# Kernel optimization log

Measured on AMD Instinct MI355X. Metric: run time of the kernel, lower is better.

Reference implementation:

```python
import jax, jax.numpy as jnp
import numpy as np

N, D, C = 4096, 512, 128
TOPK = 12  # rank-0 hard neg + up to 11 fallback ranks (torch loop breaks at loop_cnt>=10 -> max rank 11)


def setup_inputs() -> dict:
    key = jax.random.key(0)
    k1, k2, k3, k4, k5 = jax.random.split(key, 5)
    return {
        "inputs": jax.random.normal(k1, (N, D), jnp.float32),
        "prediction": jax.random.normal(k2, (N, C), jnp.float32),
        "targets": jax.random.randint(k3, (N,), 0, C),
        "true_targets": jax.random.randint(k4, (N,), 0, C),
        "prob": jax.random.uniform(k5, (N,), jnp.float32),
        "threshold": jnp.float32(0.5),
    }


def _gumbel_argmax(key, mask):
    # uniform random choice over True entries of each row (Gumbel-max trick)
    g = jax.random.gumbel(key, mask.shape, jnp.float32)
    return jnp.argmax(jnp.where(mask, g, -jnp.inf), axis=1)


def reference(inputs, prediction, targets, true_targets, prob, threshold):
    margin = jnp.float32(0.3)
    n = inputs.shape[0]
    rows = jnp.arange(n)
    # pairwise euclidean distance: ||xi||^2 + ||xj||^2 - 2 xi.xj, clamp+sqrt
    sq = jnp.sum(inputs * inputs, axis=1)
    d2 = sq[:, None] + sq[None, :] - 2.0 * (inputs @ inputs.T)
    dist = jnp.sqrt(jnp.clip(d2, 1e-12))  # [n, n]

    eye = jnp.eye(n, dtype=bool)
    same = targets[:, None] == targets[None, :]
    is_neg = ~same
    conf = prob >= threshold  # is_confident per anchor

    key = jax.random.key(42)
    kp, kp2 = jax.random.split(key)

    # random positive (!= i) and hardest negative per row
    ap_idx = _gumbel_argmax(kp, same & ~eye)
    neg_dist = jnp.where(is_neg, dist, jnp.inf)
    an_idx = jnp.argmin(neg_dist, axis=1)

    ap0 = dist[rows, ap_idx]
    an0 = dist[rows, an_idx]
    pos_conf = prob[ap_idx] >= threshold
    neg_conf = prob[an_idx] >= threshold
    # false-negative test: hard neg predicted as anchor's (noisy) label
    is_fn = jnp.argmax(prediction[an_idx], axis=1) == targets

    # case B (pos conf, neg unconf, FN): walk ranked negs for first confident one (ranks 1..11)
    nv, ni = jax.lax.top_k(-neg_dist, TOPK)  # smallest TOPK neg distances
    cand_conf = prob[ni] >= threshold
    tail = cand_conf[:, 1:]
    found = jnp.any(tail, axis=1)
    r = jnp.where(found, 1 + jnp.argmax(tail, axis=1), TOPK - 1)
    an_B = dist[rows, ni[rows, r]]

    # cases C / D-notFN: resample a confident positive (!= i); fallback to original pos
    conf_pos = same & ~eye & (prob >= threshold)[None, :]
    new_pos = jnp.where(jnp.any(conf_pos, axis=1), _gumbel_argmax(kp2, conf_pos), ap_idx)
    ap_new = dist[rows, new_pos]

    caseB = pos_conf & ~neg_conf & is_fn
    swap = (~pos_conf) & (neg_conf | ~is_fn)  # case C or case D-notFN
    inverse = (~pos_conf) & (~neg_conf) & is_fn

    half = (ap0 + an0) * 0.5
    ap = jnp.where(caseB, half, jnp.where(swap, ap_new, ap0))
    an = jnp.where(caseB, an_B, jnp.where(swap, half, an0))

    row_loss = jnp.where(inverse,
                         jax.nn.relu(an - ap + margin),
                         jax.nn.relu(ap - an + margin))
    cnt = jnp.sum(conf)
    loss = jnp.sum(jnp.where(conf, row_loss, 0.0)) / jnp.maximum(cnt, 1).astype(jnp.float32)
    correct = jnp.sum((an >= ap) & conf)
    return loss, correct
```

## Files before the change

### kernel.cpp

```cpp
#include <hip/hip_runtime.h>
#include <stdint.h>
#include <math.h>

#define N_ 4096
#define D_ 512
#define C_ 128
#define MAXC 256

typedef __attribute__((ext_vector_type(8))) short bf16x8;
typedef __attribute__((ext_vector_type(4))) float f32x4;

__host__ __device__ __forceinline__ uint32_t rotl32_(uint32_t x, int d) {
  return (x << d) | (x >> (32 - d));
}
__host__ __device__ inline void tf2x32(uint32_t k0, uint32_t k1,
                                       uint32_t x0, uint32_t x1,
                                       uint32_t& y0, uint32_t& y1) {
  const uint32_t k2 = k0 ^ k1 ^ 0x1BD11BDAu;
#define TF_R(rr) { x0 += x1; x1 = rotl32_(x1, rr); x1 ^= x0; }
  x0 += k0; x1 += k1;
  TF_R(13) TF_R(15) TF_R(26) TF_R(6)
  x0 += k1; x1 += k2 + 1u;
  TF_R(17) TF_R(29) TF_R(16) TF_R(24)
  x0 += k2; x1 += k0 + 2u;
  TF_R(13) TF_R(15) TF_R(26) TF_R(6)
  x0 += k0; x1 += k1 + 3u;
  TF_R(17) TF_R(29) TF_R(16) TF_R(24)
  x0 += k1; x1 += k2 + 4u;
  TF_R(13) TF_R(15) TF_R(26) TF_R(6)
  x0 += k2; x1 += k0 + 5u;
#undef TF_R
  y0 = x0; y1 = x1;
}

__device__ __forceinline__ float gumbel_ij(uint32_t k0, uint32_t k1, uint32_t m) {
  uint32_t y0, y1;
  tf2x32(k0, k1, 0u, m, y0, y1);
  uint32_t bits = y0 ^ y1;
  uint32_t vb = (bits >> 9) | 0x3f800000u;
  float f = __uint_as_float(vb) - 1.0f;
  float u = (f == 0.0f) ? 1.1754943508222875e-38f : f;
  return -logf(-logf(u));
}

__device__ __forceinline__ unsigned short f2bf(float x) {
  unsigned int b = __float_as_uint(x);
  b += 0x7fffu + ((b >> 16) & 1u);
  return (unsigned short)(b >> 16);
}
__device__ __forceinline__ float bf2f(unsigned short u) {
  return __uint_as_float(((unsigned int)u) << 16);
}

__global__ void zero_k(float* __restrict__ accum, int* __restrict__ ccnt) {
  int t = threadIdx.x;
  if (t == 0) {
    accum[0] = 0.0f;
    ((unsigned*)accum)[1] = 0u;
    ((unsigned*)accum)[2] = 0u;
  }
  if (t < C_) ccnt[t] = 0;
}

__global__ __launch_bounds__(64) void prep_k(const float* __restrict__ inputs,
                                             const float* __restrict__ pred,
                                             const int* __restrict__ targets,
                                             float* __restrict__ sq,
                                             int* __restrict__ pam,
                                             int* __restrict__ ccnt,
                                             int* __restrict__ clist,
                                             unsigned short* __restrict__ XH,
                                             unsigned short* __restrict__ XL,
                                             int do_split, int do_list) {
  int i = blockIdx.x;
  int lane = threadIdx.x;
  const float4* rp = (const float4*)(inputs + (size_t)i * D_);
  float s = 0.0f;
#pragma unroll
  for (int q = 0; q < 2; ++q) {
    float4 v = rp[lane + 64 * q];
    s += v.x * v.x + v.y * v.y + v.z * v.z + v.w * v.w;
    if (do_split) {
      unsigned short h0 = f2bf(v.x), h1 = f2bf(v.y), h2 = f2bf(v.z), h3 = f2bf(v.w);
      unsigned short g0 = f2bf(v.x - bf2f(h0)), g1 = f2bf(v.y - bf2f(h1));
      unsigned short g2 = f2bf(v.z - bf2f(h2)), g3 = f2bf(v.w - bf2f(h3));
      uint2 hp, lp;
      hp.x = (unsigned)h0 | ((unsigned)h1 << 16); hp.y = (unsigned)h2 | ((unsigned)h3 << 16);
      lp.x = (unsigned)g0 | ((unsigned)g1 << 16); lp.y = (unsigned)g2 | ((unsigned)g3 << 16);
      size_t blk = ((size_t)(i >> 4) * 16 + ((lane >> 3) + 8 * q)) * 512;
      int lf = (i & 15) + 16 * ((lane & 7) >> 1);
      int j0 = 4 * (lane & 1);
      *(uint2*)&XH[blk + lf * 8 + j0] = hp;
      *(uint2*)&XL[blk + lf * 8 + j0] = lp;
    }
  }
#pragma unroll
  for (int off = 32; off; off >>= 1) s += __shfl_down(s, off);
  if (lane == 0) sq[i] = s;

  float v0 = pred[(size_t)i * C_ + lane];
  float v1 = pred[(size_t)i * C_ + 64 + lane];
  float bv; int bi;
  if (v1 > v0) { bv = v1; bi = lane + 64; } else { bv = v0; bi = lane; }
#pragma unroll
  for (int off = 32; off; off >>= 1) {
    float ov = __shfl_down(bv, off);
    int oi = __shfl_down(bi, off);
    if (ov > bv || (ov == bv && oi < bi)) { bv = ov; bi = oi; }
  }
  if (lane == 0) {
    pam[i] = bi;
    if (do_list) {
      int t = targets[i];
      int p = atomicAdd(&ccnt[t], 1);
      if (p < MAXC) clist[t * MAXC + p] = i;
    }
  }
}

__global__ __launch_bounds__(256, 2) void bigk4_k(const unsigned short* __restrict__ XH,
                                                  const unsigned short* __restrict__ XL,
                                                  const int* __restrict__ targets,
                                                  const float* __restrict__ sq,
                                                  float* __restrict__ pD,
                                                  int* __restrict__ pI) {
  __shared__ float U[8448];
  __shared__ float sqc[512];
  __shared__ int tcs[512];
  __shared__ float sqr[64];
  __shared__ int trs[64];

  const int tid = threadIdx.x, w = tid >> 6, l = tid & 63;
  const int rb = blockIdx.x >> 3, sl = blockIdx.x & 7;
  const int rbase = rb * 64, cbase0 = sl * 512;

  sqc[tid] = sq[cbase0 + tid]; sqc[tid + 256] = sq[cbase0 + 256 + tid];
  tcs[tid] = targets[cbase0 + tid]; tcs[tid + 256] = targets[cbase0 + 256 + tid];
  if (tid < 64) { sqr[tid] = sq[rbase + tid]; trs[tid] = targets[rbase + tid]; }

  const int lo = l * 8;
  size_t ta[4], tb[8];
#pragma unroll
  for (int rt = 0; rt < 4; ++rt) ta[rt] = (size_t)((rbase >> 4) + rt) * 8192;
#pragma unroll
  for (int c = 0; c < 8; ++c) tb[c] = (size_t)((cbase0 >> 4) + w * 8 + c) * 8192;

  f32x4 acc[4][8];
#pragma unroll
  for (int rt = 0; rt < 4; ++rt)
#pragma unroll
    for (int c = 0; c < 8; ++c) acc[rt][c] = (f32x4){0.f, 0.f, 0.f, 0.f};

  for (int kc = 0; kc < 16; ++kc) {
    const int off = kc * 512 + lo;
    bf16x8 ah[4], al_[4];
#pragma unroll
    for (int rt = 0; rt < 4; ++rt) {
      ah[rt] = *(const bf16x8*)(XH + ta[rt] + off);
      al_[rt] = *(const bf16x8*)(XL + ta[rt] + off);
    }
#pragma unroll
    for (int c = 0; c < 8; ++c) {
      bf16x8 bh = *(const bf16x8*)(XH + tb[c] + off);
      bf16x8 bl = *(const bf16x8*)(XL + tb[c] + off);
#pragma unroll
      for (int rt = 0; rt < 4; ++rt) {
        acc[rt][c] = __builtin_amdgcn_mfma_f32_16x16x32_bf16(ah[rt], bh, acc[rt][c], 0, 0, 0);
        acc[rt][c] = __builtin_amdgcn_mfma_f32_16x16x32_bf16(ah[rt], bl, acc[rt][c], 0, 0, 0);
        acc[rt][c] = __builtin_amdgcn_mfma_f32_16x16x32_bf16(al_[rt], bh, acc[rt][c], 0, 0, 0);
      }
    }
  }

  float* Dl = U;
  float dl[12]; int il[12];
#pragma unroll
  for (int q = 0; q < 12; ++q) { dl[q] = INFINITY; il[q] = 0; }
  const int srow = tid >> 2, scq = tid & 3;
  const int orow = (l >> 4) * 4;
  const int lr = l & 15;

  for (int g = 0; g < 4; ++g) {
    __syncthreads();
    if (w == g) {
#pragma unroll
      for (int rt = 0; rt < 4; ++rt)
#pragma unroll
        for (int c = 0; c < 8; ++c)
#pragma unroll
          for (int r = 0; r < 4; ++r) {
            int row = rt * 16 + orow + r;
            int cl = c * 16 + lr;
            float d2 = sqr[row] + sqc[g * 128 + cl] - 2.0f * acc[rt][c][r];
            float d = (trs[row] == tcs[g * 128 + cl]) ? INFINITY : sqrtf(fmaxf(d2, 1e-12f));
            Dl[row * 132 + cl] = d;
          }
    }
    __syncthreads();
    for (int q = 0; q < 32; ++q) {
      float d = Dl[srow * 132 + scq + 4 * q];
      if (d < dl[11]) {
        int col = cbase0 + g * 128 + scq + 4 * q;
        bool placed = false;
#pragma unroll
        for (int t = 11; t >= 1; --t) {
          if (!placed) {
            if (dl[t - 1] > d) { dl[t] = dl[t - 1]; il[t] = il[t - 1]; }
            else { dl[t] = d; il[t] = col; placed = true; }
          }
        }
        if (!placed) { dl[0] = d; il[0] = col; }
      }
    }
  }

  __syncthreads();
  float* MD = U;
  int* MI = (int*)(U + 3072);
#pragma unroll
  for (int q = 0; q < 12; ++q) { MD[tid * 12 + q] = dl[q]; MI[tid * 12 + q] = il[q]; }
  __syncthreads();
  if ((tid & 3) == 0) {
    int row = tid >> 2;
    int grow = rbase + row;
    float* outD = pD + ((size_t)grow * 8 + sl) * 12;
    int* outI = pI + ((size_t)grow * 8 + sl) * 12;
    int p0 = 0, p1 = 0, p2 = 0, p3 = 0;
    for (int o = 0; o < 12; ++o) {
      float bd = INFINITY; int bi = 0x7fffffff; int bc = 0;
      if (p0 < 12) { float d = MD[(row * 4 + 0) * 12 + p0]; int ix = MI[(row * 4 + 0) * 12 + p0]; if (d < bd || (d == bd && ix < bi)) { bd = d; bi = ix; bc = 0; } }
      if (p1 < 12) { float d = MD[(row * 4 + 1) * 12 + p1]; int ix = MI[(row * 4 + 1) * 12 + p1]; if (d < bd || (d == bd && ix < bi)) { bd = d; bi = ix; bc = 1; } }
      if (p2 < 12) { float d = MD[(row * 4 + 2) * 12 + p2]; int ix = MI[(row * 4 + 2) * 12 + p2]; if (d < bd || (d == bd && ix < bi)) { bd = d; bi = ix; bc = 2; } }
      if (p3 < 12) { float d = MD[(row * 4 + 3) * 12 + p3]; int ix = MI[(row * 4 + 3) * 12 + p3]; if (d < bd || (d == bd && ix < bi)) { bd = d; bi = ix; bc = 3; } }
      outD[o] = bd; outI[o] = bi;
      if (bc == 0) p0++; else if (bc == 1) p1++; else if (bc == 2) p2++; else p3++;
    }
  }
}

__global__ __launch_bounds__(256, 2) void bigk_k(const float* __restrict__ inputs,
                                                 const int* __restrict__ targets,
                                                 const float* __restrict__ sq,
                                                 float* __restrict__ pD,
                                                 int* __restrict__ pI) {
  __shared__ float U[10496];
  __shared__ float sqc[256];
  __shared__ int tcs[256];
  __shared__ float sqr[64];
  __shared__ int trs[64];

  float* Al = U;
  float* Bl = U + 2176;
  float* Dl = U;
  float* MD = U;
  int* MI = (int*)(U + 3072);

  const int tid = threadIdx.x;
  const int rb = blockIdx.x >> 3, sl = blockIdx.x & 7;
  const int rbase = rb * 64, cbase0 = sl * 512;

  if (tid < 64) { sqr[tid] = sq[rbase + tid]; trs[tid] = targets[rbase + tid]; }

  float dl[12]; int il[12];
#pragma unroll
  for (int q = 0; q < 12; ++q) { dl[q] = INFINITY; il[q] = 0; }

  const int w = tid >> 6, lane = tid & 63;
  const int rg = lane >> 3, cg = lane & 7;
  const int r0 = rg * 8, c0l = w * 64 + cg * 8;
  const int srow = tid >> 2, scq = tid & 3;

  for (int ci = 0; ci < 2; ++ci) {
    const int cbase = cbase0 + ci * 256;
    __syncthreads();
    sqc[tid] = sq[cbase + tid];
    tcs[tid] = targets[cbase + tid];

    float acc[8][8];
#pragma unroll
    for (int a = 0; a < 8; ++a)
#pragma unroll
      for (int b = 0; b < 8; ++b) acc[a][b] = 0.0f;

    for (int kc = 0; kc < 16; ++kc) {
      const int kb = kc * 32;
      __syncthreads();
#pragma unroll
      for (int q = 0; q < 2; ++q) {
        int idx = tid + 256 * q;
        int row = idx >> 3, kq = idx & 7;
        float4 v = *(const float4*)(inputs + (size_t)(rbase + row) * D_ + kb + kq * 4);
        Al[(4 * kq + 0) * 68 + row] = v.x;
        Al[(4 * kq + 1) * 68 + row] = v.y;
        Al[(4 * kq + 2) * 68 + row] = v.z;
        Al[(4 * kq + 3) * 68 + row] = v.w;
      }
#pragma unroll
      for (int q = 0; q < 8; ++q) {
        int idx = tid + 256 * q;
        int col = idx >> 3, kq = idx & 7;
        float4 v = *(const float4*)(inputs + (size_t)(cbase + col) * D_ + kb + kq * 4);
        Bl[(4 * kq + 0) * 260 + col] = v.x;
        Bl[(4 * kq + 1) * 260 + col] = v.y;
        Bl[(4 * kq + 2) * 260 + col] = v.z;
        Bl[(4 * kq + 3) * 260 + col] = v.w;
      }
      __syncthreads();
#pragma unroll 4
      for (int k = 0; k < 32; ++k) {
        float4 a0 = *(const float4*)&Al[k * 68 + r0];
        float4 a1 = *(const float4*)&Al[k * 68 + r0 + 4];
        float4 b0 = *(const float4*)&Bl[k * 260 + c0l];
        float4 b1 = *(const float4*)&Bl[k * 260 + c0l + 4];
        float a_[8] = {a0.x, a0.y, a0.z, a0.w, a1.x, a1.y, a1.z, a1.w};
        float b_[8] = {b0.x, b0.y, b0.z, b0.w, b1.x, b1.y, b1.z, b1.w};
#pragma unroll
        for (int ii = 0; ii < 8; ++ii)
#pragma unroll
          for (int jj = 0; jj < 8; ++jj)
            acc[ii][jj] = fmaf(a_[ii], b_[jj], acc[ii][jj]);
      }
    }

    for (int h = 0; h < 2; ++h) {
      __syncthreads();
#pragma unroll
      for (int i = 0; i < 8; ++i) {
        float si = sqr[r0 + i];
        int ti_ = trs[r0 + i];
#pragma unroll
        for (int jj = 0; jj < 4; ++jj) {
          int j = 4 * h + jj;
          float d2 = si + sqc[c0l + j] - 2.0f * acc[i][j];
          float d = (ti_ == tcs[c0l + j]) ? INFINITY : sqrtf(fmaxf(d2, 1e-12f));
          Dl[(r0 + i) * 129 + (w * 32 + cg * 4 + jj)] = d;
        }
      }
      __syncthreads();
      for (int q = 0; q < 32; ++q) {
        float d = Dl[srow * 129 + scq * 32 + q];
        if (d < dl[11]) {
          int u = scq * 32 + q;
          int col = cbase + ((u >> 5) << 6) + (((u >> 2) & 7) << 3) + (h << 2) + (u & 3);
          bool placed = false;
#pragma unroll
          for (int t = 11; t >= 1; --t) {
            if (!placed) {
              if (dl[t - 1] > d) { dl[t] = dl[t - 1]; il[t] = il[t - 1]; }
              else { dl[t] = d; il[t] = col; placed = true; }
            }
          }
          if (!placed) { dl[0] = d; il[0] = col; }
        }
      }
    }
  }

  __syncthreads();
#pragma unroll
  for (int q = 0; q < 12; ++q) { MD[tid * 12 + q] = dl[q]; MI[tid * 12 + q] = il[q]; }
  __syncthreads();
  if ((tid & 3) == 0) {
    int row = tid >> 2;
    int grow = rbase + row;
    float* outD = pD + ((size_t)grow * 8 + sl) * 12;
    int* outI = pI + ((size_t)grow * 8 + sl) * 12;
    int p0 = 0, p1 = 0, p2 = 0, p3 = 0;
    for (int o = 0; o < 12; ++o) {
      float bd = INFINITY; int bi = 0x7fffffff; int bc = 0;
      if (p0 < 12) { float d = MD[(row * 4 + 0) * 12 + p0]; int ix = MI[(row * 4 + 0) * 12 + p0]; if (d < bd || (d == bd && ix < bi)) { bd = d; bi = ix; bc = 0; } }
      if (p1 < 12) { float d = MD[(row * 4 + 1) * 12 + p1]; int ix = MI[(row * 4 + 1) * 12 + p1]; if (d < bd || (d == bd && ix < bi)) { bd = d; bi = ix; bc = 1; } }
      if (p2 < 12) { float d = MD[(row * 4 + 2) * 12 + p2]; int ix = MI[(row * 4 + 2) * 12 + p2]; if (d < bd || (d == bd && ix < bi)) { bd = d; bi = ix; bc = 2; } }
      if (p3 < 12) { float d = MD[(row * 4 + 3) * 12 + p3]; int ix = MI[(row * 4 + 3) * 12 + p3]; if (d < bd || (d == bd && ix < bi)) { bd = d; bi = ix; bc = 3; } }
      outD[o] = bd; outI[o] = bi;
      if (bc == 0) p0++; else if (bc == 1) p1++; else if (bc == 2) p2++; else p3++;
    }
  }
}

__device__ __forceinline__ float wdist2(float4 xi0, float4 xi1,
                                        const float* __restrict__ inputs,
                                        const float* __restrict__ sq,
                                        int i, int j, int lane) {
  const float4* b = (const float4*)(inputs + (size_t)j * D_);
  float4 y0 = b[lane], y1 = b[lane + 64];
  float s = xi0.x * y0.x + xi0.y * y0.y + xi0.z * y0.z + xi0.w * y0.w +
            xi1.x * y1.x + xi1.y * y1.y + xi1.z * y1.z + xi1.w * y1.w;
#pragma unroll
  for (int off = 32; off; off >>= 1) s += __shfl_xor(s, off);
  float d2 = sq[i] + sq[j] - 2.0f * s;
  return sqrtf(fmaxf(d2, 1e-12f));
}

__global__ __launch_bounds__(256) void finalize_k(const float* __restrict__ inputs,
                                                  const int* __restrict__ targets,
                                                  const float* __restrict__ prob,
                                                  const float* __restrict__ thr_p,
                                                  const float* __restrict__ sq,
                                                  const int* __restrict__ pam,
                                                  const float* __restrict__ pD,
                                                  const int* __restrict__ pI,
                                                  const int* __restrict__ ccnt,
                                                  const int* __restrict__ clist,
                                                  float* __restrict__ accum,
                                                  uint32_t kp0, uint32_t kp1,
                                                  uint32_t kq0, uint32_t kq1,
                                                  int use_list) {
  const int wid = threadIdx.x >> 6, lane = threadIdx.x & 63;
  const int i = blockIdx.x * 4 + wid;
  const float thr = *thr_p;
  const int ti = targets[i];

  float g1 = -INFINITY; int i1 = 0;
  float g2 = -INFINITY; int i2 = 0;
  int f2 = 0;
  if (use_list) {
    int cnt = ccnt[ti]; if (cnt > MAXC) cnt = MAXC;
    const int* lst = clist + (size_t)ti * MAXC;
    for (int base = 0; base < cnt; base += 64) {
      int idx = base + lane;
      if (idx < cnt) {
        int j = lst[idx];
        if (j != i) {
          uint32_t m = ((uint32_t)i << 12) | (uint32_t)j;
          float g = gumbel_ij(kp0, kp1, m);
          if (g > g1 || (g == g1 && j < i1)) { g1 = g; i1 = j; }
          if (prob[j] >= thr) {
            float gg = gumbel_ij(kq0, kq1, m);
            if (gg > g2 || (gg == g2 && j < i2)) { g2 = gg; i2 = j; }
            f2 = 1;
          }
        }
      }
    }
  } else {
    for (int j = lane; j < N_; j += 64) {
      if (targets[j] == ti && j != i) {
        uint32_t m = ((uint32_t)i << 12) | (uint32_t)j;
        float g = gumbel_ij(kp0, kp1, m);
        if (g > g1 || (g == g1 && j < i1)) { g1 = g; i1 = j; }
        if (prob[j] >= thr) {
          float gg = gumbel_ij(kq0, kq1, m);
          if (gg > g2 || (gg == g2 && j < i2)) { g2 = gg; i2 = j; }
          f2 = 1;
        }
      }
    }
  }
#pragma unroll
  for (int off = 32; off; off >>= 1) {
    float og = __shfl_xor(g1, off); int oi = __shfl_xor(i1, off);
    if (og > g1 || (og == g1 && oi < i1)) { g1 = og; i1 = oi; }
    float oh = __shfl_xor(g2, off); int oj = __shfl_xor(i2, off);
    if (oh > g2 || (oh == g2 && oj < i2)) { g2 = oh; i2 = oj; }
  }
  f2 = __any(f2);
  const int ap_idx = i1;
  const int new_pos = f2 ? i2 : ap_idx;

  const float4* arow = (const float4*)(inputs + (size_t)i * D_);
  float4 xi0 = arow[lane], xi1 = arow[lane + 64];
  const float ap0 = wdist2(xi0, xi1, inputs, sq, i, ap_idx, lane);
  const float ap_new = wdist2(xi0, xi1, inputs, sq, i, new_pos, lane);

  const float* rowD = pD + (size_t)i * 96;
  const int* rowI = pI + (size_t)i * 96;
  int ci_[12];
  {
    int p0 = 0, p1 = 0, p2 = 0, p3 = 0, p4 = 0, p5 = 0, p6 = 0, p7 = 0;
#pragma unroll
    for (int o = 0; o < 12; ++o) {
      float bd = INFINITY; int bi = 0x7fffffff; int bs = 0;
#define HEADQ(s, ps) if (ps < 12) { float d = rowD[(s) * 12 + ps]; int ix = rowI[(s) * 12 + ps]; if (d < bd || (d == bd && ix < bi)) { bd = d; bi = ix; bs = (s); } }
      HEADQ(0, p0) HEADQ(1, p1) HEADQ(2, p2) HEADQ(3, p3)
      HEADQ(4, p4) HEADQ(5, p5) HEADQ(6, p6) HEADQ(7, p7)
#undef HEADQ
      ci_[o] = bi;
      if (bs == 0) p0++; else if (bs == 1) p1++; else if (bs == 2) p2++; else if (bs == 3) p3++;
      else if (bs == 4) p4++; else if (bs == 5) p5++; else if (bs == 6) p6++; else p7++;
    }
  }
  float de[12];
#pragma unroll
  for (int o = 0; o < 12; ++o) de[o] = wdist2(xi0, xi1, inputs, sq, i, ci_[o], lane);

  float an0 = de[0]; int an_idx = ci_[0]; int minpos = 0;
#pragma unroll
  for (int o = 1; o < 12; ++o)
    if (de[o] < an0 || (de[o] == an0 && ci_[o] < an_idx)) { an0 = de[o]; an_idx = ci_[o]; minpos = o; }
  float anB = INFINITY; int anBi = 0x7fffffff; bool fB = false;
#pragma unroll
  for (int o = 0; o < 12; ++o) {
    if (o != minpos) {
      bool cf = prob[ci_[o]] >= thr;
      if (cf && (de[o] < anB || (de[o] == anB && ci_[o] < anBi))) { anB = de[o]; anBi = ci_[o]; fB = true; }
    }
  }
  if (!fB) {
    anB = de[0]; anBi = ci_[0];
#pragma unroll
    for (int o = 1; o < 12; ++o)
      if (de[o] > anB || (de[o] == anB && ci_[o] > anBi)) { anB = de[o]; anBi = ci_[o]; }
  }
  const float an_B = anB;

  if (lane == 0) {
    bool neg_conf = prob[an_idx] >= thr;
    bool pos_conf = prob[ap_idx] >= thr;
    bool is_fn = (pam[an_idx] == ti);
    bool caseB = pos_conf && !neg_conf && is_fn;
    bool swap_ = !pos_conf && (neg_conf || !is_fn);
    bool inverse = !pos_conf && !neg_conf && is_fn;
    float half = 0.5f * (ap0 + an0);
    float ap = caseB ? half : (swap_ ? ap_new : ap0);
    float an = caseB ? an_B : (swap_ ? half : an0);
    const float margin = 0.3f;
    float rl = inverse ? fmaxf(an - ap + margin, 0.0f) : fmaxf(ap - an + margin, 0.0f);
    bool conf_i = prob[i] >= thr;
    if (conf_i) {
      atomicAdd(&accum[0], rl);
      atomicAdd(((unsigned*)accum) + 2, 1u);
      if (an >= ap) atomicAdd(((unsigned*)accum) + 1, 1u);
    }
  }
}

__global__ void writeout_k(const float* __restrict__ accum, float* __restrict__ out) {
  unsigned correct = ((const unsigned*)accum)[1];
  unsigned cnt = ((const unsigned*)accum)[2];
  out[0] = accum[0] / fmaxf((float)cnt, 1.0f);
  out[1] = (float)correct;
}

extern "C" void kernel_launch(void* const* d_in, const int* in_sizes, int n_in,
                              void* d_out, int out_size, void* d_ws, size_t ws_size,
                              hipStream_t stream) {
  const float* inputs = (const float*)d_in[0];
  const float* pred = (const float*)d_in[1];
  const int* targets = (const int*)d_in[2];
  const float* prob = (const float*)d_in[4];
  const float* thr = (const float*)d_in[5];
  float* out = (float*)d_out;

  float* sq = (float*)d_ws;
  int* pam = (int*)d_ws + N_;
  float* pD = (float*)d_ws + 2 * N_;
  int* pI = (int*)d_ws + 2 * N_ + N_ * 96;
  float* accum = (float*)d_ws + 2 * N_ + 2 * (N_ * 96);
  int* ccnt = (int*)accum + 16;
  int* clist = ccnt + C_;
  const size_t base_f = (size_t)(2 * N_ + 2 * (N_ * 96) + 16 + C_ + C_ * MAXC);
  const size_t split_off = ((base_f * 4 + 15) / 16) * 16;
  unsigned short* XH = (unsigned short*)((char*)d_ws + split_off);
  unsigned short* XL = XH + (size_t)N_ * D_;
  const size_t need = split_off + (size_t)2 * N_ * D_ * 2;
  const int use_v2 = (ws_size >= need) ? 1 : 0;

  uint32_t kp0, kp1, kq0, kq1;
  tf2x32(0u, 42u, 0u, 0u, kp0, kp1);
  tf2x32(0u, 42u, 0u, 1u, kq0, kq1);

  zero_k<<<dim3(1), dim3(128), 0, stream>>>(accum, ccnt);
  prep_k<<<dim3(N_), dim3(64), 0, stream>>>(inputs, pred, targets, sq, pam, ccnt, clist,
                                            XH, XL, use_v2, use_v2);
  if (use_v2)
    bigk4_k<<<dim3(512), dim3(256), 0, stream>>>(XH, XL, targets, sq, pD, pI);
  else
    bigk_k<<<dim3(512), dim3(256), 0, stream>>>(inputs, targets, sq, pD, pI);
  finalize_k<<<dim3(N_ / 4), dim3(256), 0, stream>>>(inputs, targets, prob, thr, sq, pam,
                                                     pD, pI, ccnt, clist, accum,
                                                     kp0, kp1, kq0, kq1, use_v2);
  writeout_k<<<dim3(1), dim3(1), 0, stream>>>(accum, out);
}
```

Before: 344.3 us.

## Stage GEMM tiles in LDS via global_load_lds and double the block size

The split-bf16 distance GEMM kernel now uses 512 threads per block. Each k-chunk is staged into shared memory with direct global-to-LDS loads, and MFMA operands are read from LDS instead of each wave reloading the row tile from global memory. Each wave now holds a 64x64 accumulator tile instead of 64x128, which lowers register pressure so more waves can be resident. In exchange there are two barriers per k-chunk with no double buffering, and the top-12 selection and merge run over 8 lanes per row instead of 4.

```diff
diff --git a/kernel.cpp b/kernel.cpp
--- a/kernel.cpp
+++ b/kernel.cpp
@@ -52,6 +52,12 @@
   return __uint_as_float(((unsigned int)u) << 16);
 }
 
+__device__ __forceinline__ void gll16(const void* g, void* lds) {
+  __builtin_amdgcn_global_load_lds(
+      (const __attribute__((address_space(1))) unsigned int*)g,
+      (__attribute__((address_space(3))) unsigned int*)lds, 16, 0, 0);
+}
+
 __global__ void zero_k(float* __restrict__ accum, int* __restrict__ ccnt) {
   int t = threadIdx.x;
   if (t == 0) {
@@ -118,56 +124,72 @@
   }
 }
 
-__global__ __launch_bounds__(256, 2) void bigk4_k(const unsigned short* __restrict__ XH,
+__global__ __launch_bounds__(512, 3) void bigk5_k(const unsigned short* __restrict__ XH,
                                                   const unsigned short* __restrict__ XL,
                                                   const int* __restrict__ targets,
                                                   const float* __restrict__ sq,
                                                   float* __restrict__ pD,
                                                   int* __restrict__ pI) {
-  __shared__ float U[8448];
+  __shared__ float U[18432];
   __shared__ float sqc[512];
   __shared__ int tcs[512];
   __shared__ float sqr[64];
   __shared__ int trs[64];
 
+  short* AH = (short*)U;
+  short* AL = AH + 2048;
+  short* BH = AH + 4096;
+  short* BL = BH + 16384;
+
   const int tid = threadIdx.x, w = tid >> 6, l = tid & 63;
   const int rb = blockIdx.x >> 3, sl = blockIdx.x & 7;
   const int rbase = rb * 64, cbase0 = sl * 512;
 
-  sqc[tid] = sq[cbase0 + tid]; sqc[tid + 256] = sq[cbase0 + 256 + tid];
-  tcs[tid] = targets[cbase0 + tid]; tcs[tid + 256] = targets[cbase0 + 256 + tid];
+  sqc[tid] = sq[cbase0 + tid];
+  tcs[tid] = targets[cbase0 + tid];
   if (tid < 64) { sqr[tid] = sq[rbase + tid]; trs[tid] = targets[rbase + tid]; }
 
   const int lo = l * 8;
-  size_t ta[4], tb[8];
-#pragma unroll
-  for (int rt = 0; rt < 4; ++rt) ta[rt] = (size_t)((rbase >> 4) + rt) * 8192;
-#pragma unroll
-  for (int c = 0; c < 8; ++c) tb[c] = (size_t)((cbase0 >> 4) + w * 8 + c) * 8192;
-
-  f32x4 acc[4][8];
+  const size_t taw = (size_t)((rbase >> 4) + (w >> 1)) * 8192;
+  const size_t tb0 = (size_t)((cbase0 >> 4) + w * 4) * 8192;
+
+  f32x4 acc[4][4];
 #pragma unroll
   for (int rt = 0; rt < 4; ++rt)
 #pragma unroll
-    for (int c = 0; c < 8; ++c) acc[rt][c] = (f32x4){0.f, 0.f, 0.f, 0.f};
+    for (int c = 0; c < 4; ++c) acc[rt][c] = (f32x4){0.f, 0.f, 0.f, 0.f};
 
   for (int kc = 0; kc < 16; ++kc) {
     const int off = kc * 512 + lo;
-    bf16x8 ah[4], al_[4];
+    __syncthreads();
+    {
+      const unsigned short* sp = (w & 1) ? XL : XH;
+      short* dp = ((w & 1) ? AL : AH) + (w >> 1) * 512;
+      gll16(sp + taw + off, dp);
+    }
+#pragma unroll
+    for (int c = 0; c < 4; ++c) {
+      size_t tb = tb0 + (size_t)c * 8192 + off;
+      gll16(XH + tb, BH + (w * 4 + c) * 512);
+      gll16(XL + tb, BL + (w * 4 + c) * 512);
+    }
+    __syncthreads();
+
+    bf16x8 ah[4], am[4];
 #pragma unroll
     for (int rt = 0; rt < 4; ++rt) {
-      ah[rt] = *(const bf16x8*)(XH + ta[rt] + off);
-      al_[rt] = *(const bf16x8*)(XL + ta[rt] + off);
-    }
-#pragma unroll
-    for (int c = 0; c < 8; ++c) {
-      bf16x8 bh = *(const bf16x8*)(XH + tb[c] + off);
-      bf16x8 bl = *(const bf16x8*)(XL + tb[c] + off);
+      ah[rt] = *(const bf16x8*)(AH + rt * 512 + lo);
+      am[rt] = *(const bf16x8*)(AL + rt * 512 + lo);
+    }
+#pragma unroll
+    for (int c = 0; c < 4; ++c) {
+      bf16x8 bh = *(const bf16x8*)(BH + (w * 4 + c) * 512 + lo);
+      bf16x8 bl = *(const bf16x8*)(BL + (w * 4 + c) * 512 + lo);
 #pragma unroll
       for (int rt = 0; rt < 4; ++rt) {
         acc[rt][c] = __builtin_amdgcn_mfma_f32_16x16x32_bf16(ah[rt], bh, acc[rt][c], 0, 0, 0);
         acc[rt][c] = __builtin_amdgcn_mfma_f32_16x16x32_bf16(ah[rt], bl, acc[rt][c], 0, 0, 0);
-        acc[rt][c] = __builtin_amdgcn_mfma_f32_16x16x32_bf16(al_[rt], bh, acc[rt][c], 0, 0, 0);
+        acc[rt][c] = __builtin_amdgcn_mfma_f32_16x16x32_bf16(am[rt], bh, acc[rt][c], 0, 0, 0);
       }
     }
   }
@@ -176,31 +198,32 @@
   float dl[12]; int il[12];
 #pragma unroll
   for (int q = 0; q < 12; ++q) { dl[q] = INFINITY; il[q] = 0; }
-  const int srow = tid >> 2, scq = tid & 3;
-  const int orow = (l >> 4) * 4;
-  const int lr = l & 15;
-
-  for (int g = 0; g < 4; ++g) {
+  const int srow = tid >> 3, u0 = tid & 7;
+  const int orow = (l >> 4) * 4, lr = l & 15;
+
+  for (int g = 0; g < 8; ++g) {
     __syncthreads();
     if (w == g) {
 #pragma unroll
       for (int rt = 0; rt < 4; ++rt)
 #pragma unroll
-        for (int c = 0; c < 8; ++c)
+        for (int c = 0; c < 4; ++c)
 #pragma unroll
           for (int r = 0; r < 4; ++r) {
             int row = rt * 16 + orow + r;
             int cl = c * 16 + lr;
-            float d2 = sqr[row] + sqc[g * 128 + cl] - 2.0f * acc[rt][c][r];
-            float d = (trs[row] == tcs[g * 128 + cl]) ? INFINITY : sqrtf(fmaxf(d2, 1e-12f));
-            Dl[row * 132 + cl] = d;
+            float d2 = sqr[row] + sqc[g * 64 + cl] - 2.0f * acc[rt][c][r];
+            float d = (trs[row] == tcs[g * 64 + cl]) ? INFINITY : sqrtf(fmaxf(d2, 1e-12f));
+            Dl[row * 68 + cl] = d;
           }
     }
     __syncthreads();
-    for (int q = 0; q < 32; ++q) {
-      float d = Dl[srow * 132 + scq + 4 * q];
+#pragma unroll
+    for (int q = 0; q < 8; ++q) {
+      int u = u0 + 8 * q;
+      float d = Dl[srow * 68 + u];
       if (d < dl[11]) {
-        int col = cbase0 + g * 128 + scq + 4 * q;
+        int col = cbase0 + g * 64 + u;
         bool placed = false;
 #pragma unroll
         for (int t = 11; t >= 1; --t) {
@@ -216,24 +239,25 @@
 
   __syncthreads();
   float* MD = U;
-  int* MI = (int*)(U + 3072);
+  int* MI = (int*)(U + 6144);
 #pragma unroll
   for (int q = 0; q < 12; ++q) { MD[tid * 12 + q] = dl[q]; MI[tid * 12 + q] = il[q]; }
   __syncthreads();
-  if ((tid & 3) == 0) {
-    int row = tid >> 2;
+  if ((tid & 7) == 0) {
+    int row = tid >> 3;
     int grow = rbase + row;
     float* outD = pD + ((size_t)grow * 8 + sl) * 12;
     int* outI = pI + ((size_t)grow * 8 + sl) * 12;
-    int p0 = 0, p1 = 0, p2 = 0, p3 = 0;
+    int p0 = 0, p1 = 0, p2 = 0, p3 = 0, p4 = 0, p5 = 0, p6 = 0, p7 = 0;
     for (int o = 0; o < 12; ++o) {
-      float bd = INFINITY; int bi = 0x7fffffff; int bc = 0;
-      if (p0 < 12) { float d = MD[(row * 4 + 0) * 12 + p0]; int ix = MI[(row * 4 + 0) * 12 + p0]; if (d < bd || (d == bd && ix < bi)) { bd = d; bi = ix; bc = 0; } }
-      if (p1 < 12) { float d = MD[(row * 4 + 1) * 12 + p1]; int ix = MI[(row * 4 + 1) * 12 + p1]; if (d < bd || (d == bd && ix < bi)) { bd = d; bi = ix; bc = 1; } }
-      if (p2 < 12) { float d = MD[(row * 4 + 2) * 12 + p2]; int ix = MI[(row * 4 + 2) * 12 + p2]; if (d < bd || (d == bd && ix < bi)) { bd = d; bi = ix; bc = 2; } }
-      if (p3 < 12) { float d = MD[(row * 4 + 3) * 12 + p3]; int ix = MI[(row * 4 + 3) * 12 + p3]; if (d < bd || (d == bd && ix < bi)) { bd = d; bi = ix; bc = 3; } }
+      float bd = INFINITY; int bi = 0x7fffffff; int bs = 0;
+#define HEADM(s, ps) if (ps < 12) { float d = MD[(row * 8 + (s)) * 12 + ps]; int ix = MI[(row * 8 + (s)) * 12 + ps]; if (d < bd || (d == bd && ix < bi)) { bd = d; bi = ix; bs = (s); } }
+      HEADM(0, p0) HEADM(1, p1) HEADM(2, p2) HEADM(3, p3)
+      HEADM(4, p4) HEADM(5, p5) HEADM(6, p6) HEADM(7, p7)
+#undef HEADM
       outD[o] = bd; outI[o] = bi;
-      if (bc == 0) p0++; else if (bc == 1) p1++; else if (bc == 2) p2++; else p3++;
+      if (bs == 0) p0++; else if (bs == 1) p1++; else if (bs == 2) p2++; else if (bs == 3) p3++;
+      else if (bs == 4) p4++; else if (bs == 5) p5++; else if (bs == 6) p6++; else p7++;
     }
   }
 }
@@ -564,7 +588,7 @@
   prep_k<<<dim3(N_), dim3(64), 0, stream>>>(inputs, pred, targets, sq, pam, ccnt, clist,
                                             XH, XL, use_v2, use_v2);
   if (use_v2)
-    bigk4_k<<<dim3(512), dim3(256), 0, stream>>>(XH, XL, targets, sq, pD, pI);
+    bigk5_k<<<dim3(512), dim3(512), 0, stream>>>(XH, XL, targets, sq, pD, pI);
   else
     bigk_k<<<dim3(512), dim3(256), 0, stream>>>(inputs, targets, sq, pD, pI);
   finalize_k<<<dim3(N_ / 4), dim3(256), 0, stream>>>(inputs, targets, prob, thr, sq, pam,
```

Result: slower. 394.2 us (+14.5%).
